# Kernel optimization log

Hardware: AMD Instinct MI355X
Metric: run time of the kernel (lower is better)

## Reference

```python
import jax, jax.numpy as jnp
import numpy as np

B, T, F, H, L = 16384, 24, 7, 8, 4
DENSE = [T * H, 1024, 2048, 4]


def setup_inputs() -> dict:
    key = jax.random.key(0)
    d = {"x": jax.random.normal(jax.random.fold_in(key, 0), (B, T, F), jnp.float32)}
    k = 1
    s = 1.0 / np.sqrt(H)  # torch LSTM init bound
    for l in range(L):
        in_dim = F if l == 0 else H
        for name, shape in [("Wih", (4 * H, in_dim)), ("Whh", (4 * H, H)), ("bih", (4 * H,)), ("bhh", (4 * H,))]:
            d[f"{name}{l}"] = jax.random.uniform(jax.random.fold_in(key, k), shape, jnp.float32, -s, s)
            k += 1
    for i in range(1, len(DENSE)):
        si = 1.0 / np.sqrt(DENSE[i - 1])
        d[f"Wd{i}"] = jax.random.uniform(jax.random.fold_in(key, k), (DENSE[i], DENSE[i - 1]), jnp.float32, -si, si)
        k += 1
        d[f"bd{i}"] = jax.random.uniform(jax.random.fold_in(key, k), (DENSE[i],), jnp.float32, -si, si)
        k += 1
    return d


def _lstm_layer(xs, Wih, Whh, b):
    # xs: [T, B, in] -> ys: [T, B, H]; torch gate order i,f,g,o
    Hn = Whh.shape[1]
    h0 = jnp.zeros((xs.shape[1], Hn), xs.dtype)

    def step(carry, xt):
        h, c = carry
        z = xt @ Wih.T + h @ Whh.T + b  # [B, 4H]
        i, f, g, o = jnp.split(z, 4, axis=-1)
        c = jax.nn.sigmoid(f) * c + jax.nn.sigmoid(i) * jnp.tanh(g)
        h = jax.nn.sigmoid(o) * jnp.tanh(c)
        return (h, c), h

    (_, _), ys = jax.lax.scan(step, (h0, h0), xs)
    return ys


def _forward(x, lstm_params, dense_params):
    xs = jnp.transpose(x, (1, 0, 2))  # [T, B, F]
    for (Wih, Whh, bih, bhh) in lstm_params:
        xs = _lstm_layer(xs, Wih, Whh, bih + bhh)
    out = jnp.transpose(xs, (1, 0, 2)).reshape(x.shape[0], T * H)  # [B, 192]
    (W1, b1), (W2, b2), (W3, b3) = dense_params
    out = jax.nn.relu(out @ W1.T + b1)
    out = jax.nn.relu(out @ W2.T + b2)
    return out @ W3.T + b3  # [B, num_classes]


def reference(x, Wih0, Whh0, bih0, bhh0, Wih1, Whh1, bih1, bhh1, Wih2, Whh2, bih2, bhh2, Wih3, Whh3, bih3, bhh3, Wd1, bd1, Wd2, bd2, Wd3, bd3):
    lstm_params = [(Wih0, Whh0, bih0, bhh0), (Wih1, Whh1, bih1, bhh1), (Wih2, Whh2, bih2, bhh2), (Wih3, Whh3, bih3, bhh3)]
    dense_params = [(Wd1, bd1), (Wd2, bd2), (Wd3, bd3)]
    return _forward(x, lstm_params, dense_params)
```

## Files before the change

kernel.cpp:

```cpp
#include <hip/hip_runtime.h>
#include <hip/hip_bf16.h>

typedef __attribute__((ext_vector_type(4))) float f32x4;
typedef __attribute__((ext_vector_type(16))) float f32x16;
typedef __attribute__((ext_vector_type(2))) float f32x2;
typedef __attribute__((ext_vector_type(8))) short bf16x8;

__device__ __forceinline__ ushort f2bf(float f) {
    union { float f; uint u; } v; v.f = f;
    uint u = v.u;
    return (ushort)((u + 0x7fffu + ((u >> 16) & 1u)) >> 16);
}
__device__ __forceinline__ float sigm(float x) {
    return __builtin_amdgcn_rcpf(1.0f + __builtin_amdgcn_exp2f(x * -1.442695040888963f));
}
__device__ __forceinline__ float tanh_(float x) {
    return 2.0f * __builtin_amdgcn_rcpf(1.0f + __builtin_amdgcn_exp2f(x * -2.885390081777927f)) - 1.0f;
}

typedef const __attribute__((address_space(1))) unsigned int ga_u32;
typedef __attribute__((address_space(3))) unsigned int lds_u32;
__device__ __forceinline__ void g2l16(const void* g, void* l) {
    __builtin_amdgcn_global_load_lds((ga_u32*)(unsigned long long)g,
                                     (lds_u32*)(unsigned int)(unsigned long long)l,
                                     16, 0, 0);
}

struct LstmW {
    const float* wih[4];
    const float* whh[4];
    const float* bih[4];
    const float* bhh[4];
};

__device__ __forceinline__ void gates8p(const f32x2 w01[8], const f32x2 w23[8],
                                        const float xv8[8], f32x2& a01, f32x2& a23) {
#pragma unroll
    for (int k = 0; k < 8; ++k) {
        f32x2 xv = {xv8[k], xv8[k]};
        a01 += w01[k] * xv;
        a23 += w23[k] * xv;
    }
}
__device__ __forceinline__ void cellup(f32x2 a01, f32x2 a23, float& h, float& c) {
    c = sigm(a01.y) * c + sigm(a01.x) * tanh_(a23.x);
    h = sigm(a23.y) * tanh_(c);
}
__device__ __forceinline__ void ld8(const float* p, float v[8]) {
    float4 a = *(const float4*)p;
    float4 b = *(const float4*)(p + 4);
    v[0] = a.x; v[1] = a.y; v[2] = a.z; v[3] = a.w;
    v[4] = b.x; v[5] = b.y; v[6] = b.z; v[7] = b.w;
}

__global__ __launch_bounds__(256) void pre_kernel(const float* __restrict__ x, LstmW p,
                                                  ushort* __restrict__ Y,
                                                  const float* __restrict__ W1,
                                                  const float* __restrict__ W2,
                                                  ushort* __restrict__ W1b,
                                                  ushort* __restrict__ W2b,
                                                  const float* __restrict__ b3,
                                                  float* __restrict__ out) {
    __shared__ float xs[32 * 168];
    __shared__ float hb[32 * 200];

    const int tid = threadIdx.x;
    if (blockIdx.x >= 512) {
        const int tg = (blockIdx.x - 512) * 256 + tid;
        if (tg < 16384) {
            float4 bv = {b3[0], b3[1], b3[2], b3[3]};
            ((float4*)out)[tg] = bv;
        }
#pragma unroll
        for (int s = 0; s < 4; ++s) {
            int i = tg + s * 143360;
            const float4* src; ushort4* dst; int off;
            if (i < 49152) { src = (const float4*)W1; dst = (ushort4*)W1b; off = i; }
            else { src = (const float4*)W2; dst = (ushort4*)W2b; off = i - 49152; }
            float4 v = src[off];
            ushort4 r; r.x = f2bf(v.x); r.y = f2bf(v.y); r.z = f2bf(v.z); r.w = f2bf(v.w);
            dst[off] = r;
        }
        return;
    }

    const int e0 = blockIdx.x * 32;
    {
        const float4* s = (const float4*)(x + (size_t)e0 * 168);
        float4* d = (float4*)xs;
        for (int i = tid; i < 1344; i += 256) d[i] = s[i];
    }
    __syncthreads();

    const int el = tid >> 3, j = tid & 7;
    float* hr = hb + el * 200;
    const float* xr = xs + el * 168;

    f32x2 wx01[8], wx23[8], wh01[8], wh23[8], b01, b23;

    {
        const float* Wih = p.wih[0];
        const float* Whh = p.whh[0];
#pragma unroll
        for (int k = 0; k < 7; ++k) {
            wx01[k] = {Wih[(0 + j) * 7 + k], Wih[(8 + j) * 7 + k]};
            wx23[k] = {Wih[(16 + j) * 7 + k], Wih[(24 + j) * 7 + k]};
        }
#pragma unroll
        for (int k = 0; k < 8; ++k) {
            wh01[k] = {Whh[(0 + j) * 8 + k], Whh[(8 + j) * 8 + k]};
            wh23[k] = {Whh[(16 + j) * 8 + k], Whh[(24 + j) * 8 + k]};
        }
        b01 = {p.bih[0][j] + p.bhh[0][j], p.bih[0][8 + j] + p.bhh[0][8 + j]};
        b23 = {p.bih[0][16 + j] + p.bhh[0][16 + j], p.bih[0][24 + j] + p.bhh[0][24 + j]};

        float h = 0.f, c = 0.f;
        {
            f32x2 a01 = b01, a23 = b23;
#pragma unroll
            for (int k = 0; k < 7; ++k) {
                f32x2 xv = {xr[k], xr[k]};
                a01 += wx01[k] * xv; a23 += wx23[k] * xv;
            }
            cellup(a01, a23, h, c);
            hr[j] = h;
        }
        for (int t = 1; t < 24; ++t) {
            f32x2 a01 = b01, a23 = b23;
#pragma unroll
            for (int k = 0; k < 7; ++k) {
                f32x2 xv = {xr[t * 7 + k], xr[t * 7 + k]};
                a01 += wx01[k] * xv; a23 += wx23[k] * xv;
            }
            float hp[8]; ld8(&hr[(t - 1) * 8], hp);
            gates8p(wh01, wh23, hp, a01, a23);
            cellup(a01, a23, h, c);
            hr[t * 8 + j] = h;
        }
    }

#pragma unroll
    for (int l = 1; l < 4; ++l) {
        const float* Wih = p.wih[l];
        const float* Whh = p.whh[l];
#pragma unroll
        for (int k = 0; k < 8; ++k) {
            wx01[k] = {Wih[(0 + j) * 8 + k], Wih[(8 + j) * 8 + k]};
            wx23[k] = {Wih[(16 + j) * 8 + k], Wih[(24 + j) * 8 + k]};
            wh01[k] = {Whh[(0 + j) * 8 + k], Whh[(8 + j) * 8 + k]};
            wh23[k] = {Whh[(16 + j) * 8 + k], Whh[(24 + j) * 8 + k]};
        }
        b01 = {p.bih[l][j] + p.bhh[l][j], p.bih[l][8 + j] + p.bhh[l][8 + j]};
        b23 = {p.bih[l][16 + j] + p.bhh[l][16 + j], p.bih[l][24 + j] + p.bhh[l][24 + j]};

        float h = 0.f, c = 0.f;
        {
            float xin[8]; ld8(&hr[0], xin);
            f32x2 a01 = b01, a23 = b23;
            gates8p(wx01, wx23, xin, a01, a23);
            cellup(a01, a23, h, c);
            hr[j] = h;
            if (l == 3) Y[((size_t)(e0 + el) * 24) * 8 + j] = f2bf(h);
        }
        for (int t = 1; t < 24; ++t) {
            float xin[8]; ld8(&hr[t * 8], xin);
            float hp[8];  ld8(&hr[(t - 1) * 8], hp);
            f32x2 a01 = b01, a23 = b23;
            gates8p(wx01, wx23, xin, a01, a23);
            gates8p(wh01, wh23, hp, a01, a23);
            cellup(a01, a23, h, c);
            hr[t * 8 + j] = h;
            if (l == 3) Y[((size_t)(e0 + el) * 24 + t) * 8 + j] = f2bf(h);
        }
    }
}

template <int KDIM, bool FUSE3>
__device__ __forceinline__ void gemm_body(const ushort* __restrict__ A,
                                          const ushort* __restrict__ W,
                                          const float* __restrict__ bias,
                                          ushort* __restrict__ Hout,
                                          const float* __restrict__ W3,
                                          float* __restrict__ outf, int N) {
    constexpr int SMEMN = FUSE3 ? 16896 : 16384;
    __shared__ alignas(16) ushort smem[SMEMN];
    __shared__ alignas(16) float w3s[FUSE3 ? 528 : 1];
    ushort* As = smem;
    ushort* Ws = smem + 8192;

    const int tid = threadIdx.x;
    const int m0 = blockIdx.x * 128;
    const int n0 = blockIdx.y * 128;
    const int lane = tid & 63;
    const int wv = tid >> 6;
    const int wm = (wv & 1) * 64;
    const int wn = (wv >> 1) * 64;
    const int l31 = lane & 31;
    const int kh = lane >> 5;

    if (FUSE3) {
        for (int i = tid; i < 512; i += 256)
            w3s[(i >> 7) * 132 + (i & 127)] = W3[(size_t)(i >> 7) * 2048 + n0 + (i & 127)];
    }

    const int lrow = lane >> 3;
    const int lchunk = (lane & 7) ^ lrow;
    const ushort* Ag = A + (size_t)(m0 + wv * 32 + lrow) * KDIM + lchunk * 8;
    const ushort* Wg = W + (size_t)(n0 + wv * 32 + lrow) * KDIM + lchunk * 8;
    ushort* Ald = As + wv * 2048;
    ushort* Wld = Ws + wv * 2048;

    const int r7 = l31 & 7;
    const int arow0 = (wm + l31) * 64;
    const int brow0 = (wn + l31) * 64;

    f32x16 acc[2][2];
#pragma unroll
    for (int mi = 0; mi < 2; ++mi)
#pragma unroll
        for (int ni = 0; ni < 2; ++ni)
#pragma unroll
            for (int r = 0; r < 16; ++r) acc[mi][ni][r] = 0.f;

    for (int k0 = 0; k0 < KDIM; k0 += 64) {
#pragma unroll
        for (int c = 0; c < 4; ++c)
            g2l16(Ag + (size_t)c * 8 * KDIM + k0, Ald + c * 512);
#pragma unroll
        for (int c = 0; c < 4; ++c)
            g2l16(Wg + (size_t)c * 8 * KDIM + k0, Wld + c * 512);
        __syncthreads();

#pragma unroll
        for (int ks = 0; ks < 4; ++ks) {
            const int ck = ((ks * 2 + kh) ^ r7) * 8;
            bf16x8 afr[2], bfr[2];
#pragma unroll
            for (int mi = 0; mi < 2; ++mi)
                afr[mi] = *(const bf16x8*)&As[arow0 + mi * 2048 + ck];
#pragma unroll
            for (int ni = 0; ni < 2; ++ni)
                bfr[ni] = *(const bf16x8*)&Ws[brow0 + ni * 2048 + ck];
#pragma unroll
            for (int mi = 0; mi < 2; ++mi)
#pragma unroll
                for (int ni = 0; ni < 2; ++ni)
                    acc[mi][ni] = __builtin_amdgcn_mfma_f32_32x32x16_bf16(afr[mi], bfr[ni],
                                                                         acc[mi][ni], 0, 0, 0);
        }
        __syncthreads();
    }

    if (!FUSE3) {
#pragma unroll
        for (int ni = 0; ni < 2; ++ni) {
            const int col = n0 + wn + ni * 32 + l31;
            const float b = bias[col];
#pragma unroll
            for (int mi = 0; mi < 2; ++mi)
#pragma unroll
                for (int r = 0; r < 16; ++r) {
                    const int row = m0 + wm + mi * 32 + (r & 3) + 8 * (r >> 2) + 4 * kh;
                    Hout[(size_t)row * N + col] = f2bf(fmaxf(acc[mi][ni][r] + b, 0.f));
                }
        }
    } else {
        float* Cs = (float*)smem;
        const int drow = tid >> 2;
        const int dn = tid & 3;
#pragma unroll
        for (int pass = 0; pass < 2; ++pass) {
            if ((wv & 1) == pass) {
#pragma unroll
                for (int ni = 0; ni < 2; ++ni) {
                    const int cl = wn + ni * 32 + l31;
                    const float b = bias[n0 + cl];
#pragma unroll
                    for (int mi = 0; mi < 2; ++mi)
#pragma unroll
                        for (int r = 0; r < 16; ++r) {
                            const int rl = mi * 32 + (r & 3) + 8 * (r >> 2) + 4 * kh;
                            Cs[rl * 132 + cl] = fmaxf(acc[mi][ni][r] + b, 0.f);
                        }
                }
            }
            __syncthreads();
            const float* crow = &Cs[drow * 132];
            const float* wrow = &w3s[dn * 132];
            float p = 0.f;
#pragma unroll
            for (int ch = 0; ch < 32; ++ch) {
                f32x4 cv = *(const f32x4*)(crow + ch * 4);
                f32x4 wv4 = *(const f32x4*)(wrow + ch * 4);
                p += cv[0] * wv4[0] + cv[1] * wv4[1] + cv[2] * wv4[2] + cv[3] * wv4[3];
            }
            atomicAdd(&outf[(size_t)(m0 + pass * 64 + drow) * 4 + dn], p);
            __syncthreads();
        }
    }
}

__global__ __launch_bounds__(256, 4) void gemm1_kernel(const ushort* __restrict__ A,
                                                       const ushort* __restrict__ W,
                                                       const float* __restrict__ bias,
                                                       ushort* __restrict__ Hout, int N) {
    gemm_body<192, false>(A, W, bias, Hout, nullptr, nullptr, N);
}
__global__ __launch_bounds__(256, 4) void gemm2_kernel(const ushort* __restrict__ A,
                                                       const ushort* __restrict__ W,
                                                       const float* __restrict__ bias,
                                                       const float* __restrict__ W3,
                                                       float* __restrict__ outf) {
    gemm_body<1024, true>(A, W, bias, nullptr, W3, outf, 2048);
}

extern "C" void kernel_launch(void* const* d_in, const int* in_sizes, int n_in,
                              void* d_out, int out_size, void* d_ws, size_t ws_size,
                              hipStream_t stream) {
    const float* x = (const float*)d_in[0];
    LstmW w;
    for (int l = 0; l < 4; ++l) {
        w.wih[l] = (const float*)d_in[1 + 4 * l];
        w.whh[l] = (const float*)d_in[2 + 4 * l];
        w.bih[l] = (const float*)d_in[3 + 4 * l];
        w.bhh[l] = (const float*)d_in[4 + 4 * l];
    }
    const float* Wd1 = (const float*)d_in[17];
    const float* bd1 = (const float*)d_in[18];
    const float* Wd2 = (const float*)d_in[19];
    const float* bd2 = (const float*)d_in[20];
    const float* Wd3 = (const float*)d_in[21];
    const float* bd3 = (const float*)d_in[22];
    float* out = (float*)d_out;

    ushort* Y   = (ushort*)d_ws;
    ushort* H1  = (ushort*)((char*)d_ws + 6291456);
    ushort* W1b = (ushort*)((char*)d_ws + 39845888);
    ushort* W2b = (ushort*)((char*)d_ws + 40239104);

    pre_kernel<<<1072, 256, 0, stream>>>(x, w, Y, Wd1, Wd2, W1b, W2b, bd3, out);
    gemm1_kernel<<<dim3(128, 8), 256, 0, stream>>>(Y, W1b, bd1, H1, 1024);
    gemm2_kernel<<<dim3(128, 16), 256, 0, stream>>>(H1, W2b, bd2, Wd3, out);
}
```

Measured before the change: 225.6 us.

## Double-buffer GEMM LDS tiles with K=32 stages and prefetch next tile

The dense GEMM main loop now uses two LDS buffers of K=32 tiles, issuing the global-to-LDS loads for the next stage before computing on the current one. Only one barrier per iteration remains. The swizzle pattern and row stride are adapted to the 32-wide tile. This hides global load latency behind the MFMA work. In exchange, each barrier now covers half as much compute per iteration, and the LDS reuse pattern changes.

```diff
diff --git a/kernel.cpp b/kernel.cpp
--- a/kernel.cpp
+++ b/kernel.cpp
@@ -185,8 +185,6 @@
     constexpr int SMEMN = FUSE3 ? 16896 : 16384;
     __shared__ alignas(16) ushort smem[SMEMN];
     __shared__ alignas(16) float w3s[FUSE3 ? 528 : 1];
-    ushort* As = smem;
-    ushort* Ws = smem + 8192;
 
     const int tid = threadIdx.x;
     const int m0 = blockIdx.x * 128;
@@ -203,16 +201,16 @@
             w3s[(i >> 7) * 132 + (i & 127)] = W3[(size_t)(i >> 7) * 2048 + n0 + (i & 127)];
     }
 
-    const int lrow = lane >> 3;
-    const int lchunk = (lane & 7) ^ lrow;
-    const ushort* Ag = A + (size_t)(m0 + wv * 32 + lrow) * KDIM + lchunk * 8;
-    const ushort* Wg = W + (size_t)(n0 + wv * 32 + lrow) * KDIM + lchunk * 8;
-    ushort* Ald = As + wv * 2048;
-    ushort* Wld = Ws + wv * 2048;
-
-    const int r7 = l31 & 7;
-    const int arow0 = (wm + l31) * 64;
-    const int brow0 = (wn + l31) * 64;
+    const int srow = lane >> 2;
+    const int schunk = (lane & 3) ^ ((lane >> 3) & 3);
+    const ushort* Ag = A + (size_t)(m0 + wv * 32 + srow) * KDIM + schunk * 8;
+    const ushort* Wg = W + (size_t)(n0 + wv * 32 + srow) * KDIM + schunk * 8;
+    const int ldsA = wv * 1024;
+    const int ldsW = 4096 + wv * 1024;
+
+    const int swz = (l31 >> 1) & 3;
+    const int arow0 = (wm + l31) * 32;
+    const int brow0 = (wn + l31) * 32;
 
     f32x16 acc[2][2];
 #pragma unroll
@@ -222,25 +220,38 @@
 #pragma unroll
             for (int r = 0; r < 16; ++r) acc[mi][ni][r] = 0.f;
 
-    for (int k0 = 0; k0 < KDIM; k0 += 64) {
-#pragma unroll
-        for (int c = 0; c < 4; ++c)
-            g2l16(Ag + (size_t)c * 8 * KDIM + k0, Ald + c * 512);
-#pragma unroll
-        for (int c = 0; c < 4; ++c)
-            g2l16(Wg + (size_t)c * 8 * KDIM + k0, Wld + c * 512);
+#pragma unroll
+    for (int c = 0; c < 2; ++c) {
+        g2l16(Ag + (size_t)c * 16 * KDIM, smem + ldsA + c * 512);
+        g2l16(Wg + (size_t)c * 16 * KDIM, smem + ldsW + c * 512);
+    }
+
+    constexpr int ITERS = KDIM / 32;
+#pragma unroll 2
+    for (int it = 0; it < ITERS; ++it) {
         __syncthreads();
-
-#pragma unroll
-        for (int ks = 0; ks < 4; ++ks) {
-            const int ck = ((ks * 2 + kh) ^ r7) * 8;
+        const int cur = (it & 1) * 8192;
+        if (it + 1 < ITERS) {
+            const int nxt = ((it + 1) & 1) * 8192;
+            const int k1 = (it + 1) * 32;
+#pragma unroll
+            for (int c = 0; c < 2; ++c) {
+                g2l16(Ag + (size_t)c * 16 * KDIM + k1, smem + nxt + ldsA + c * 512);
+                g2l16(Wg + (size_t)c * 16 * KDIM + k1, smem + nxt + ldsW + c * 512);
+            }
+        }
+        const ushort* As = smem + cur;
+        const ushort* Ws = smem + cur + 4096;
+#pragma unroll
+        for (int ks = 0; ks < 2; ++ks) {
+            const int ck = ((ks * 2 + kh) ^ swz) * 8;
             bf16x8 afr[2], bfr[2];
 #pragma unroll
             for (int mi = 0; mi < 2; ++mi)
-                afr[mi] = *(const bf16x8*)&As[arow0 + mi * 2048 + ck];
+                afr[mi] = *(const bf16x8*)&As[arow0 + mi * 1024 + ck];
 #pragma unroll
             for (int ni = 0; ni < 2; ++ni)
-                bfr[ni] = *(const bf16x8*)&Ws[brow0 + ni * 2048 + ck];
+                bfr[ni] = *(const bf16x8*)&Ws[brow0 + ni * 1024 + ck];
 #pragma unroll
             for (int mi = 0; mi < 2; ++mi)
 #pragma unroll
@@ -248,8 +259,8 @@
                     acc[mi][ni] = __builtin_amdgcn_mfma_f32_32x32x16_bf16(afr[mi], bfr[ni],
                                                                          acc[mi][ni], 0, 0, 0);
         }
-        __syncthreads();
-    }
+    }
+    __syncthreads();
 
     if (!FUSE3) {
 #pragma unroll
```

Result: slower. 231.1 us (+2.4%).
